# Performance work log

Measured on AMD Instinct MI355X. Metric: run time of the kernel, lower is better.

Reference implementation:

```python
import jax, jax.numpy as jnp
import numpy as np

FLOW_NUM = 2048
H = 64  # lstm_output_dim
NOISE_DIM = 3


def _w(key, shape, s=0.08):
    return (jax.random.normal(key, shape, dtype=jnp.float32) * s)


def setup_inputs() -> dict:
    key = jax.random.key(0)
    ks = jax.random.split(key, 20)
    d = {
        "noise": jax.random.normal(ks[0], (FLOW_NUM, NOISE_DIM), dtype=jnp.float32),
        "w_ih0": _w(ks[1], (4 * H, NOISE_DIM)),
        "w_hh0": _w(ks[2], (4 * H, H)),
        "b_ih0": _w(ks[3], (4 * H,)),
        "b_hh0": _w(ks[4], (4 * H,)),
        "w_ih1": _w(ks[5], (4 * H, H)),
        "w_hh1": _w(ks[6], (4 * H, H)),
        "b_ih1": _w(ks[7], (4 * H,)),
        "b_hh1": _w(ks[8], (4 * H,)),
        "w_ih2": _w(ks[9], (4 * H, H)),
        "w_hh2": _w(ks[10], (4 * H, H)),
        "b_ih2": _w(ks[11], (4 * H,)),
        "b_hh2": _w(ks[12], (4 * H,)),
        "fc1_w": _w(ks[13], (32, H)),
        "fc1_b": _w(ks[14], (32,)),
        "fc2_w": _w(ks[15], (16, 32)),
        "fc2_b": _w(ks[16], (16,)),
        "fc3_w": _w(ks[17], (3, 16)),
        "fc3_b": _w(ks[18], (3,)),
        "flow_length": 500,
    }
    return d


def _lstm_cell(x, h, c, w_ih, w_hh, b_ih, b_hh):
    # PyTorch gate order: input, forget, cell(g), output
    gates = x @ w_ih.T + h @ w_hh.T + (b_ih + b_hh)
    i, f, g, o = jnp.split(gates, 4, axis=-1)
    c_new = jax.nn.sigmoid(f) * c + jax.nn.sigmoid(i) * jnp.tanh(g)
    h_new = jax.nn.sigmoid(o) * jnp.tanh(c_new)
    return h_new, c_new


def reference(noise, w_ih0, w_hh0, b_ih0, b_hh0,
              w_ih1, w_hh1, b_ih1, b_hh1,
              w_ih2, w_hh2, b_ih2, b_hh2,
              fc1_w, fc1_b, fc2_w, fc2_b, fc3_w, fc3_b,
              flow_length):
    layers = [(w_ih0, w_hh0, b_ih0, b_hh0),
              (w_ih1, w_hh1, b_ih1, b_hh1),
              (w_ih2, w_hh2, b_ih2, b_hh2)]
    n = noise.shape[0]
    h0 = jnp.zeros((3, n, H), dtype=noise.dtype)
    c0 = jnp.zeros((3, n, H), dtype=noise.dtype)

    def step(carry, _):
        x, h, c = carry
        inp = x
        hs, cs = [], []
        for l, (wi, wh, bi, bh) in enumerate(layers):
            h_l, c_l = _lstm_cell(inp, h[l], c[l], wi, wh, bi, bh)
            hs.append(h_l)
            cs.append(c_l)
            inp = h_l
        # MLP head (Dropout is identity in eval mode); LeakyReLU slope 0.01
        y = jax.nn.leaky_relu(inp @ fc1_w.T + fc1_b)
        y = jax.nn.leaky_relu(y @ fc2_w.T + fc2_b)
        y = jax.nn.leaky_relu(y @ fc3_w.T + fc3_b)
        return (y, jnp.stack(hs), jnp.stack(cs)), y

    _, flow = jax.lax.scan(step, (noise, h0, c0), None, length=flow_length)
    # flow: [flow_length, flow_num, 3] -> [flow_num, flow_length, 3]
    return jnp.swapaxes(flow, 0, 1)
```

## Files before the change

### kernel.cpp

```cpp
#include <hip/hip_runtime.h>

#define NT 512

typedef _Float16 f16x8 __attribute__((ext_vector_type(8)));
typedef _Float16 f16x4 __attribute__((ext_vector_type(4)));
typedef float    f32x4 __attribute__((ext_vector_type(4)));

#define MFMA(a, b, c) __builtin_amdgcn_mfma_f32_16x16x32_f16((a), (b), (c), 0, 0, 0)

#if __has_builtin(__builtin_amdgcn_exp2f)
__device__ __forceinline__ float fexp(float x) { return __builtin_amdgcn_exp2f(x * 1.4426950408889634f); }
#else
__device__ __forceinline__ float fexp(float x) { return __expf(x); }
#endif
#if __has_builtin(__builtin_amdgcn_rcpf)
__device__ __forceinline__ float frcp(float x) { return __builtin_amdgcn_rcpf(x); }
#else
__device__ __forceinline__ float frcp(float x) { return 1.0f / x; }
#endif
__device__ __forceinline__ float sigm(float x)  { return frcp(1.0f + fexp(-x)); }
__device__ __forceinline__ float tanh_(float x) { return 1.0f - 2.0f * frcp(1.0f + fexp(2.0f * x)); }
__device__ __forceinline__ float lrelu(float x) { return x > 0.0f ? x : 0.01f * x; }

__device__ __forceinline__ f16x8 ld8(const float* p) {
    const float4* q = (const float4*)p;
    float4 a = q[0], b = q[1];
    f16x8 r = { (_Float16)a.x, (_Float16)a.y, (_Float16)a.z, (_Float16)a.w,
                (_Float16)b.x, (_Float16)b.y, (_Float16)b.z, (_Float16)b.w };
    return r;
}

__global__ __launch_bounds__(NT, 2)
void gen_kernel(
    const float* __restrict__ noise,
    const float* __restrict__ w_ih0, const float* __restrict__ w_hh0,
    const float* __restrict__ b_ih0, const float* __restrict__ b_hh0,
    const float* __restrict__ w_ih1, const float* __restrict__ w_hh1,
    const float* __restrict__ b_ih1, const float* __restrict__ b_hh1,
    const float* __restrict__ w_ih2, const float* __restrict__ w_hh2,
    const float* __restrict__ b_ih2, const float* __restrict__ b_hh2,
    const float* __restrict__ fc1_w, const float* __restrict__ fc1_b,
    const float* __restrict__ fc2_w, const float* __restrict__ fc2_b,
    const float* __restrict__ fc3_w, const float* __restrict__ fc3_b,
    const int*   __restrict__ flow_len_p,
    float* __restrict__ out)
{
    __shared__ _Float16 sh[3][2][16 * 64] __attribute__((aligned(16)));
    __shared__ _Float16 sx [16][40] __attribute__((aligned(16)));
    __shared__ _Float16 sy1[16][40] __attribute__((aligned(16)));
    __shared__ _Float16 sy2[16][40] __attribute__((aligned(16)));

    const int tid  = threadIdx.x;
    const int l    = tid & 63;
    const int w    = tid >> 6;
    const int ls   = l & 15;
    const int lj   = l >> 4;
    const int base = blockIdx.x * 8;
    const int T    = flow_len_p[0];

    const int gA  = ls & 3;
    const int rA0 = gA * 64 + 4 * (2 * w + 0) + (ls >> 2);
    const int rA1 = gA * 64 + 4 * (2 * w + 1) + (ls >> 2);

    f16x8 A1[2][4], A2[2][4], A0[2][3];
#pragma unroll
    for (int kc = 0; kc < 2; ++kc) {
        A1[0][kc]     = ld8(w_ih1 + rA0 * 64 + 32 * kc + 8 * lj);
        A1[1][kc]     = ld8(w_ih1 + rA1 * 64 + 32 * kc + 8 * lj);
        A1[0][2 + kc] = ld8(w_hh1 + rA0 * 64 + 32 * kc + 8 * lj);
        A1[1][2 + kc] = ld8(w_hh1 + rA1 * 64 + 32 * kc + 8 * lj);
        A2[0][kc]     = ld8(w_ih2 + rA0 * 64 + 32 * kc + 8 * lj);
        A2[1][kc]     = ld8(w_ih2 + rA1 * 64 + 32 * kc + 8 * lj);
        A2[0][2 + kc] = ld8(w_hh2 + rA0 * 64 + 32 * kc + 8 * lj);
        A2[1][2 + kc] = ld8(w_hh2 + rA1 * 64 + 32 * kc + 8 * lj);
        A0[0][kc]     = ld8(w_hh0 + rA0 * 64 + 32 * kc + 8 * lj);
        A0[1][kc]     = ld8(w_hh0 + rA1 * 64 + 32 * kc + 8 * lj);
    }
#pragma unroll
    for (int tt = 0; tt < 2; ++tt) {
        const int r = tt ? rA1 : rA0;
        f16x8 v;
#pragma unroll
        for (int i = 0; i < 8; ++i) {
            int kl = 8 * lj + i;
            float x = (kl < 3) ? w_ih0[r * 3 + kl]
                    : (kl == 3) ? (b_ih0[r] + b_hh0[r]) : 0.0f;
            v[i] = (_Float16)x;
        }
        A0[tt][2] = v;
    }
    f16x8 F1[2][2], F2, F3;
#pragma unroll
    for (int tt = 0; tt < 2; ++tt)
#pragma unroll
        for (int kc = 0; kc < 2; ++kc)
            F1[tt][kc] = ld8(fc1_w + (16 * tt + ls) * 64 + 32 * kc + 8 * lj);
    F2 = ld8(fc2_w + ls * 32 + 8 * lj);
    {
        f16x8 v;
#pragma unroll
        for (int i = 0; i < 8; ++i) {
            int k = 8 * lj + i;
            v[i] = (_Float16)((ls < 3 && k < 16) ? fc3_w[ls * 16 + k] : 0.0f);
        }
        F3 = v;
    }
    const int uc0 = 8 * w + lj, uc1 = 8 * w + 4 + lj;
    const int u_own = (ls < 8) ? uc0 : uc1;
    const int cs    = ls & 7;
    const int whaddr = cs * 64 + 8 * (((u_own >> 3) + cs) & 7) + (u_own & 7);
    float b1o[4], b2o[4];
#pragma unroll
    for (int g = 0; g < 4; ++g) {
        b1o[g] = b_ih1[g * 64 + u_own] + b_hh1[g * 64 + u_own];
        b2o[g] = b_ih2[g * 64 + u_own] + b_hh2[g * 64 + u_own];
    }
    float hb1a[4], hb1b[4], hb2[4];
#pragma unroll
    for (int r = 0; r < 4; ++r) {
        hb1a[r] = fc1_b[4 * lj + r];
        hb1b[r] = fc1_b[16 + 4 * lj + r];
        hb2[r]  = fc2_b[4 * lj + r];
    }
    float fb3[3] = { fc3_b[0], fc3_b[1], fc3_b[2] };

    for (int i = tid; i < 3 * 2 * 16 * 64; i += NT) ((_Float16*)sh)[i] = (_Float16)0.0f;
    for (int i = tid; i < 16 * 40; i += NT) {
        ((_Float16*)sx)[i]  = (_Float16)0.0f;
        ((_Float16*)sy1)[i] = (_Float16)0.0f;
        ((_Float16*)sy2)[i] = (_Float16)0.0f;
    }
    __syncthreads();
    if (tid < 16) sx[tid][3] = (_Float16)1.0f;
    if (tid < 24) {
        int s = tid / 3, d = tid % 3;
        sx[s][d] = (_Float16)noise[(base + s) * 3 + d];
    }

    float c0s = 0.0f, c1s = 0.0f, c2s = 0.0f;
    const float zb[4] = {0, 0, 0, 0};
    __syncthreads();

#define RD(L, p, kg) (*(const f16x8*)&sh[L][p][ls * 64 + 8 * (((kg) + ls) & 7)])

#define REPACK(cell, a0, a1)                                                   \
    float cell[4];                                                             \
    _Pragma("unroll")                                                          \
    for (int r = 0; r < 4; ++r) {                                              \
        float v_ = __shfl_xor(a1[r], 8);                                       \
        cell[r] = (ls < 8) ? a0[r] : v_;                                       \
    }

#define ACTC(cell, bo, cref, L, p) {                                           \
        float gi = cell[0] + bo[0], gf = cell[1] + bo[1];                      \
        float gg = cell[2] + bo[2], go = cell[3] + bo[3];                      \
        cref = sigm(gf) * cref + sigm(gi) * tanh_(gg);                         \
        sh[L][p][whaddr] = (_Float16)(sigm(go) * tanh_(cref)); }

    {
        f16x8 bx = *(const f16x8*)&sx[ls][8 * lj];
        f32x4 a0 = {0, 0, 0, 0}, a1 = {0, 0, 0, 0};
        a0 = MFMA(A0[0][2], bx, a0);
        a1 = MFMA(A0[1][2], bx, a1);
        REPACK(cell, a0, a1)
        ACTC(cell, zb, c0s, 0, 0)
    }
    __syncthreads();
    f16x8 ph1a = RD(1, 1, lj), ph1b = RD(1, 1, 4 + lj);

    for (int t = 0; t < T; ++t) {
        const int pc = t & 1, pp = pc ^ 1;
        f16x8 r0 = RD(0, pc, lj), r1 = RD(0, pc, 4 + lj);
        f16x8 nh2a = RD(2, pp, lj), nh2b = RD(2, pp, 4 + lj);
        {
            f32x4 a0 = {0, 0, 0, 0}, a1 = {0, 0, 0, 0};
            a0 = MFMA(A1[0][0], r0, a0);   a1 = MFMA(A1[1][0], r0, a1);
            a0 = MFMA(A1[0][1], r1, a0);   a1 = MFMA(A1[1][1], r1, a1);
            a0 = MFMA(A1[0][2], ph1a, a0); a1 = MFMA(A1[1][2], ph1a, a1);
            a0 = MFMA(A1[0][3], ph1b, a0); a1 = MFMA(A1[1][3], ph1b, a1);
            REPACK(cell, a0, a1)
            ACTC(cell, b1o, c1s, 1, pc)
        }
        __syncthreads();
        {
            f16x8 s0 = RD(1, pc, lj), s1 = RD(1, pc, 4 + lj);
            f32x4 a0 = {0, 0, 0, 0}, a1 = {0, 0, 0, 0};
            a0 = MFMA(A2[0][0], s0, a0);   a1 = MFMA(A2[1][0], s0, a1);
            a0 = MFMA(A2[0][1], s1, a0);   a1 = MFMA(A2[1][1], s1, a1);
            a0 = MFMA(A2[0][2], nh2a, a0); a1 = MFMA(A2[1][2], nh2a, a1);
            a0 = MFMA(A2[0][3], nh2b, a0); a1 = MFMA(A2[1][3], nh2b, a1);
            REPACK(cell, a0, a1)
            ACTC(cell, b2o, c2s, 2, pc)
        }
        __syncthreads();
        f32x4 h0a = {0, 0, 0, 0}, h0b = {0, 0, 0, 0};
        h0a = MFMA(A0[0][0], r0, h0a); h0b = MFMA(A0[1][0], r0, h0b);
        h0a = MFMA(A0[0][1], r1, h0a); h0b = MFMA(A0[1][1], r1, h0b);
        if (w == 0) {
            f16x8 bh0 = RD(2, pc, lj), bh1 = RD(2, pc, 4 + lj);
            f32x4 y1a = {0, 0, 0, 0}, y1b = {0, 0, 0, 0};
            y1a = MFMA(F1[0][0], bh0, y1a); y1b = MFMA(F1[1][0], bh0, y1b);
            y1a = MFMA(F1[0][1], bh1, y1a); y1b = MFMA(F1[1][1], bh1, y1b);
            f16x4 v;
#pragma unroll
            for (int r = 0; r < 4; ++r) v[r] = (_Float16)lrelu(y1a[r] + hb1a[r]);
            *(f16x4*)&sy1[ls][4 * lj] = v;
#pragma unroll
            for (int r = 0; r < 4; ++r) v[r] = (_Float16)lrelu(y1b[r] + hb1b[r]);
            *(f16x4*)&sy1[ls][16 + 4 * lj] = v;
            f16x8 by1 = *(const f16x8*)&sy1[ls][8 * lj];
            f32x4 y2 = {0, 0, 0, 0};
            y2 = MFMA(F2, by1, y2);
#pragma unroll
            for (int r = 0; r < 4; ++r) v[r] = (_Float16)lrelu(y2[r] + hb2[r]);
            *(f16x4*)&sy2[ls][4 * lj] = v;
            f16x8 by2 = *(const f16x8*)&sy2[ls][8 * lj];
            f32x4 y3 = {0, 0, 0, 0};
            y3 = MFMA(F3, by2, y3);
            if (lj == 0) {
                float o0 = lrelu(y3[0] + fb3[0]);
                float o1 = lrelu(y3[1] + fb3[1]);
                float o2 = lrelu(y3[2] + fb3[2]);
                sx[ls][0] = (_Float16)o0;
                sx[ls][1] = (_Float16)o1;
                sx[ls][2] = (_Float16)o2;
                if (ls < 8) {
                    float* op = out + ((size_t)(base + ls) * T + t) * 3;
                    op[0] = o0; op[1] = o1; op[2] = o2;
                }
            }
        }
        __syncthreads();
        {
            f16x8 bx = *(const f16x8*)&sx[ls][8 * lj];
            h0a = MFMA(A0[0][2], bx, h0a);
            h0b = MFMA(A0[1][2], bx, h0b);
            REPACK(cell, h0a, h0b)
            ACTC(cell, zb, c0s, 0, pp)
        }
        ph1a = RD(1, pc, lj); ph1b = RD(1, pc, 4 + lj);
        __syncthreads();
    }
}

extern "C" void kernel_launch(void* const* d_in, const int* in_sizes, int n_in,
                              void* d_out, int out_size, void* d_ws, size_t ws_size,
                              hipStream_t stream) {
    const float* noise = (const float*)d_in[0];
    const float* w_ih0 = (const float*)d_in[1];
    const float* w_hh0 = (const float*)d_in[2];
    const float* b_ih0 = (const float*)d_in[3];
    const float* b_hh0 = (const float*)d_in[4];
    const float* w_ih1 = (const float*)d_in[5];
    const float* w_hh1 = (const float*)d_in[6];
    const float* b_ih1 = (const float*)d_in[7];
    const float* b_hh1 = (const float*)d_in[8];
    const float* w_ih2 = (const float*)d_in[9];
    const float* w_hh2 = (const float*)d_in[10];
    const float* b_ih2 = (const float*)d_in[11];
    const float* b_hh2 = (const float*)d_in[12];
    const float* fc1w  = (const float*)d_in[13];
    const float* fc1b  = (const float*)d_in[14];
    const float* fc2w  = (const float*)d_in[15];
    const float* fc2b  = (const float*)d_in[16];
    const float* fc3w  = (const float*)d_in[17];
    const float* fc3b  = (const float*)d_in[18];
    const int*   flp   = (const int*)d_in[19];

    gen_kernel<<<dim3(256), dim3(NT), 0, stream>>>(
        noise, w_ih0, w_hh0, b_ih0, b_hh0,
        w_ih1, w_hh1, b_ih1, b_hh1,
        w_ih2, w_hh2, b_ih2, b_hh2,
        fc1w, fc1b, fc2w, fc2b, fc3w, fc3b,
        flp, (float*)d_out);
}
```

Measured before the change: 808.3 us.

## Replace MLP head LDS round-trips with cross-lane shuffles and unroll time loop by two

The MLP head on wave 0 used to write its fc1 and fc2 activations to shared memory and read them back as MFMA B-operands. That is now done with packed half shuffles inside the wave, so the sy1/sy2 buffers go away. The time loop is unrolled by two so the ping-pong buffer indices are constant, and the rotated LDS addresses are computed once before the loop. This removes LDS latency from the serial head path at the cost of shuffle instructions and larger code.

```diff
diff --git a/kernel.cpp b/kernel.cpp
--- a/kernel.cpp
+++ b/kernel.cpp
@@ -3,7 +3,6 @@
 #define NT 512
 
 typedef _Float16 f16x8 __attribute__((ext_vector_type(8)));
-typedef _Float16 f16x4 __attribute__((ext_vector_type(4)));
 typedef float    f32x4 __attribute__((ext_vector_type(4)));
 
 #define MFMA(a, b, c) __builtin_amdgcn_mfma_f32_16x16x32_f16((a), (b), (c), 0, 0, 0)
@@ -28,6 +27,13 @@
     f16x8 r = { (_Float16)a.x, (_Float16)a.y, (_Float16)a.z, (_Float16)a.w,
                 (_Float16)b.x, (_Float16)b.y, (_Float16)b.z, (_Float16)b.w };
     return r;
+}
+__device__ __forceinline__ unsigned pack2(float a, float b) {
+    union { _Float16 h[2]; unsigned u; } x;
+    x.h[0] = (_Float16)a; x.h[1] = (_Float16)b; return x.u;
+}
+__device__ __forceinline__ _Float16 half_of(unsigned v, int sel) {
+    union { unsigned u; _Float16 h[2]; } x; x.u = v; return x.h[sel];
 }
 
 __global__ __launch_bounds__(NT, 2)
@@ -46,9 +52,7 @@
     float* __restrict__ out)
 {
     __shared__ _Float16 sh[3][2][16 * 64] __attribute__((aligned(16)));
-    __shared__ _Float16 sx [16][40] __attribute__((aligned(16)));
-    __shared__ _Float16 sy1[16][40] __attribute__((aligned(16)));
-    __shared__ _Float16 sy2[16][40] __attribute__((aligned(16)));
+    __shared__ _Float16 sx[16][40] __attribute__((aligned(16)));
 
     const int tid  = threadIdx.x;
     const int l    = tid & 63;
@@ -124,12 +128,15 @@
     }
     float fb3[3] = { fc3_b[0], fc3_b[1], fc3_b[2] };
 
+    const int colb = ls * 64;
+    const int rot0 = colb + 8 * ((lj + ls) & 7);
+    const int rot1 = colb + 8 * ((4 + lj + ls) & 7);
+    const int sxoff = ls * 40 + 8 * lj;
+    const int laneA = ls + 32 * (lj & 1);
+    const int selH  = lj >> 1;
+
     for (int i = tid; i < 3 * 2 * 16 * 64; i += NT) ((_Float16*)sh)[i] = (_Float16)0.0f;
-    for (int i = tid; i < 16 * 40; i += NT) {
-        ((_Float16*)sx)[i]  = (_Float16)0.0f;
-        ((_Float16*)sy1)[i] = (_Float16)0.0f;
-        ((_Float16*)sy2)[i] = (_Float16)0.0f;
-    }
+    for (int i = tid; i < 16 * 40; i += NT) ((_Float16*)sx)[i] = (_Float16)0.0f;
     __syncthreads();
     if (tid < 16) sx[tid][3] = (_Float16)1.0f;
     if (tid < 24) {
@@ -141,7 +148,7 @@
     const float zb[4] = {0, 0, 0, 0};
     __syncthreads();
 
-#define RD(L, p, kg) (*(const f16x8*)&sh[L][p][ls * 64 + 8 * (((kg) + ls) & 7)])
+#define RDo(L, p, off) (*(const f16x8*)&sh[L][p][off])
 
 #define REPACK(cell, a0, a1)                                                   \
     float cell[4];                                                             \
@@ -158,7 +165,7 @@
         sh[L][p][whaddr] = (_Float16)(sigm(go) * tanh_(cref)); }
 
     {
-        f16x8 bx = *(const f16x8*)&sx[ls][8 * lj];
+        f16x8 bx = *(const f16x8*)((const _Float16*)sx + sxoff);
         f32x4 a0 = {0, 0, 0, 0}, a1 = {0, 0, 0, 0};
         a0 = MFMA(A0[0][2], bx, a0);
         a1 = MFMA(A0[1][2], bx, a1);
@@ -166,80 +173,105 @@
         ACTC(cell, zb, c0s, 0, 0)
     }
     __syncthreads();
-    f16x8 ph1a = RD(1, 1, lj), ph1b = RD(1, 1, 4 + lj);
-
-    for (int t = 0; t < T; ++t) {
-        const int pc = t & 1, pp = pc ^ 1;
-        f16x8 r0 = RD(0, pc, lj), r1 = RD(0, pc, 4 + lj);
-        f16x8 nh2a = RD(2, pp, lj), nh2b = RD(2, pp, 4 + lj);
-        {
-            f32x4 a0 = {0, 0, 0, 0}, a1 = {0, 0, 0, 0};
-            a0 = MFMA(A1[0][0], r0, a0);   a1 = MFMA(A1[1][0], r0, a1);
-            a0 = MFMA(A1[0][1], r1, a0);   a1 = MFMA(A1[1][1], r1, a1);
-            a0 = MFMA(A1[0][2], ph1a, a0); a1 = MFMA(A1[1][2], ph1a, a1);
-            a0 = MFMA(A1[0][3], ph1b, a0); a1 = MFMA(A1[1][3], ph1b, a1);
-            REPACK(cell, a0, a1)
-            ACTC(cell, b1o, c1s, 1, pc)
+    f16x8 ph1a = RDo(1, 1, rot0), ph1b = RDo(1, 1, rot1);
+
+#define STEPBODY(PC, PP, tt)                                                   \
+    {                                                                          \
+                                                                       \
+        f16x8 r0 = RDo(0, PC, rot0), r1 = RDo(0, PC, rot1);                    \
+        f16x8 nh2a = RDo(2, PP, rot0), nh2b = RDo(2, PP, rot1);                \
+        {                                                                      \
+            f32x4 a0 = {0, 0, 0, 0}, a1 = {0, 0, 0, 0};                        \
+            a0 = MFMA(A1[0][0], r0, a0);   a1 = MFMA(A1[1][0], r0, a1);        \
+            a0 = MFMA(A1[0][1], r1, a0);   a1 = MFMA(A1[1][1], r1, a1);        \
+            a0 = MFMA(A1[0][2], ph1a, a0); a1 = MFMA(A1[1][2], ph1a, a1);      \
+            a0 = MFMA(A1[0][3], ph1b, a0); a1 = MFMA(A1[1][3], ph1b, a1);      \
+            REPACK(cell, a0, a1)                                               \
+            ACTC(cell, b1o, c1s, 1, PC)                                        \
+        }                                                                      \
+        __syncthreads();                                                       \
+                                                                       \
+        {                                                                      \
+            f16x8 s0 = RDo(1, PC, rot0), s1 = RDo(1, PC, rot1);                \
+            f32x4 a0 = {0, 0, 0, 0}, a1 = {0, 0, 0, 0};                        \
+            a0 = MFMA(A2[0][0], s0, a0);   a1 = MFMA(A2[1][0], s0, a1);        \
+            a0 = MFMA(A2[0][1], s1, a0);   a1 = MFMA(A2[1][1], s1, a1);        \
+            a0 = MFMA(A2[0][2], nh2a, a0); a1 = MFMA(A2[1][2], nh2a, a1);      \
+            a0 = MFMA(A2[0][3], nh2b, a0); a1 = MFMA(A2[1][3], nh2b, a1);      \
+            REPACK(cell, a0, a1)                                               \
+            ACTC(cell, b2o, c2s, 2, PC)                                        \
+        }                                                                      \
+        __syncthreads();                                                       \
+              \
+        f32x4 h0a = {0, 0, 0, 0}, h0b = {0, 0, 0, 0};                          \
+        h0a = MFMA(A0[0][0], r0, h0a); h0b = MFMA(A0[1][0], r0, h0b);          \
+        h0a = MFMA(A0[0][1], r1, h0a); h0b = MFMA(A0[1][1], r1, h0b);          \
+        if (w == 0) {                                                          \
+            f16x8 bh0 = RDo(2, PC, rot0), bh1 = RDo(2, PC, rot1);              \
+            f32x4 y1a = {0, 0, 0, 0}, y1b = {0, 0, 0, 0};                      \
+            y1a = MFMA(F1[0][0], bh0, y1a); y1b = MFMA(F1[1][0], bh0, y1b);    \
+            y1a = MFMA(F1[0][1], bh1, y1a); y1b = MFMA(F1[1][1], bh1, y1b);    \
+            unsigned pk[4];                                                    \
+            _Pragma("unroll")                                                  \
+            for (int r = 0; r < 4; ++r)                                        \
+                pk[r] = pack2(lrelu(y1a[r] + hb1a[r]),                         \
+                              lrelu(y1b[r] + hb1b[r]));                        \
+            f16x8 by1;                                                         \
+            _Pragma("unroll")                                                  \
+            for (int i = 0; i < 4; ++i)                                        \
+                by1[i] = half_of((unsigned)__shfl((int)pk[i], laneA), selH);   \
+            _Pragma("unroll")                                                  \
+            for (int i = 0; i < 4; ++i)                                        \
+                by1[4 + i] = half_of((unsigned)__shfl((int)pk[i], laneA + 16), selH); \
+            f32x4 y2 = {0, 0, 0, 0};                                           \
+            y2 = MFMA(F2, by1, y2);                                            \
+            float y2r[4];                                                      \
+            _Pragma("unroll")                                                  \
+            for (int r = 0; r < 4; ++r) y2r[r] = lrelu(y2[r] + hb2[r]);        \
+            f16x8 by2;                                                         \
+            _Pragma("unroll")                                                  \
+            for (int i = 0; i < 4; ++i) {                                      \
+                float v_ = __shfl(y2r[i], laneA);                              \
+                by2[i] = (lj < 2) ? (_Float16)v_ : (_Float16)0.0f;             \
+            }                                                                  \
+            _Pragma("unroll")                                                  \
+            for (int i = 0; i < 4; ++i) {                                      \
+                float v_ = __shfl(y2r[i], laneA + 16);                         \
+                by2[4 + i] = (lj < 2) ? (_Float16)v_ : (_Float16)0.0f;         \
+            }                                                                  \
+            f32x4 y3 = {0, 0, 0, 0};                                           \
+            y3 = MFMA(F3, by2, y3);                                            \
+            if (lj == 0) {                                                     \
+                float o0 = lrelu(y3[0] + fb3[0]);                              \
+                float o1 = lrelu(y3[1] + fb3[1]);                              \
+                float o2 = lrelu(y3[2] + fb3[2]);                              \
+                sx[ls][0] = (_Float16)o0;                                      \
+                sx[ls][1] = (_Float16)o1;                                      \
+                sx[ls][2] = (_Float16)o2;                                      \
+                if (ls < 8) {                                                  \
+                    float* op = out + ((size_t)(base + ls) * T + (tt)) * 3;    \
+                    op[0] = o0; op[1] = o1; op[2] = o2;                        \
+                }                                                              \
+            }                                                                  \
+        }                                                                      \
+        __syncthreads();                                                       \
+                                                                       \
+        {                                                                      \
+            f16x8 bx = *(const f16x8*)((const _Float16*)sx + sxoff);           \
+            h0a = MFMA(A0[0][2], bx, h0a);                                     \
+            h0b = MFMA(A0[1][2], bx, h0b);                                     \
+            REPACK(cell, h0a, h0b)                                             \
+            ACTC(cell, zb, c0s, 0, PP)                                         \
+        }                                                                      \
+        ph1a = RDo(1, PC, rot0); ph1b = RDo(1, PC, rot1);                      \
+        __syncthreads();                                                       \
+    }
+
+    for (int t = 0; t < T; t += 2) {
+        STEPBODY(0, 1, t)
+        if (t + 1 < T) {
+            STEPBODY(1, 0, t + 1)
         }
-        __syncthreads();
-        {
-            f16x8 s0 = RD(1, pc, lj), s1 = RD(1, pc, 4 + lj);
-            f32x4 a0 = {0, 0, 0, 0}, a1 = {0, 0, 0, 0};
-            a0 = MFMA(A2[0][0], s0, a0);   a1 = MFMA(A2[1][0], s0, a1);
-            a0 = MFMA(A2[0][1], s1, a0);   a1 = MFMA(A2[1][1], s1, a1);
-            a0 = MFMA(A2[0][2], nh2a, a0); a1 = MFMA(A2[1][2], nh2a, a1);
-            a0 = MFMA(A2[0][3], nh2b, a0); a1 = MFMA(A2[1][3], nh2b, a1);
-            REPACK(cell, a0, a1)
-            ACTC(cell, b2o, c2s, 2, pc)
-        }
-        __syncthreads();
-        f32x4 h0a = {0, 0, 0, 0}, h0b = {0, 0, 0, 0};
-        h0a = MFMA(A0[0][0], r0, h0a); h0b = MFMA(A0[1][0], r0, h0b);
-        h0a = MFMA(A0[0][1], r1, h0a); h0b = MFMA(A0[1][1], r1, h0b);
-        if (w == 0) {
-            f16x8 bh0 = RD(2, pc, lj), bh1 = RD(2, pc, 4 + lj);
-            f32x4 y1a = {0, 0, 0, 0}, y1b = {0, 0, 0, 0};
-            y1a = MFMA(F1[0][0], bh0, y1a); y1b = MFMA(F1[1][0], bh0, y1b);
-            y1a = MFMA(F1[0][1], bh1, y1a); y1b = MFMA(F1[1][1], bh1, y1b);
-            f16x4 v;
-#pragma unroll
-            for (int r = 0; r < 4; ++r) v[r] = (_Float16)lrelu(y1a[r] + hb1a[r]);
-            *(f16x4*)&sy1[ls][4 * lj] = v;
-#pragma unroll
-            for (int r = 0; r < 4; ++r) v[r] = (_Float16)lrelu(y1b[r] + hb1b[r]);
-            *(f16x4*)&sy1[ls][16 + 4 * lj] = v;
-            f16x8 by1 = *(const f16x8*)&sy1[ls][8 * lj];
-            f32x4 y2 = {0, 0, 0, 0};
-            y2 = MFMA(F2, by1, y2);
-#pragma unroll
-            for (int r = 0; r < 4; ++r) v[r] = (_Float16)lrelu(y2[r] + hb2[r]);
-            *(f16x4*)&sy2[ls][4 * lj] = v;
-            f16x8 by2 = *(const f16x8*)&sy2[ls][8 * lj];
-            f32x4 y3 = {0, 0, 0, 0};
-            y3 = MFMA(F3, by2, y3);
-            if (lj == 0) {
-                float o0 = lrelu(y3[0] + fb3[0]);
-                float o1 = lrelu(y3[1] + fb3[1]);
-                float o2 = lrelu(y3[2] + fb3[2]);
-                sx[ls][0] = (_Float16)o0;
-                sx[ls][1] = (_Float16)o1;
-                sx[ls][2] = (_Float16)o2;
-                if (ls < 8) {
-                    float* op = out + ((size_t)(base + ls) * T + t) * 3;
-                    op[0] = o0; op[1] = o1; op[2] = o2;
-                }
-            }
-        }
-        __syncthreads();
-        {
-            f16x8 bx = *(const f16x8*)&sx[ls][8 * lj];
-            h0a = MFMA(A0[0][2], bx, h0a);
-            h0b = MFMA(A0[1][2], bx, h0b);
-            REPACK(cell, h0a, h0b)
-            ACTC(cell, zb, c0s, 0, pp)
-        }
-        ph1a = RD(1, pc, lj); ph1b = RD(1, pc, 4 + lj);
-        __syncthreads();
     }
 }
 
```

After: 865.4 us. 1.07x slower.

## Compute MLP head redundantly in every wave and drop a block barrier

Applied to the files above, without the earlier changes.

Each wave now computes the fc1/fc2/fc3 head itself, where before only wave 0 did it and passed results through shared memory. The layer outputs move between lanes with cross-lane shuffles instead of LDS staging. This removes one __syncthreads per timestep plus the sx/sy1/sy2 shared buffers, shortening the serial critical path of the recurrence. In exchange every wave repeats the head MFMAs and shuffles, which adds per-wave work.

```diff
diff --git a/kernel.cpp b/kernel.cpp
--- a/kernel.cpp
+++ b/kernel.cpp
@@ -3,7 +3,6 @@
 #define NT 512
 
 typedef _Float16 f16x8 __attribute__((ext_vector_type(8)));
-typedef _Float16 f16x4 __attribute__((ext_vector_type(4)));
 typedef float    f32x4 __attribute__((ext_vector_type(4)));
 
 #define MFMA(a, b, c) __builtin_amdgcn_mfma_f32_16x16x32_f16((a), (b), (c), 0, 0, 0)
@@ -28,6 +27,13 @@
     f16x8 r = { (_Float16)a.x, (_Float16)a.y, (_Float16)a.z, (_Float16)a.w,
                 (_Float16)b.x, (_Float16)b.y, (_Float16)b.z, (_Float16)b.w };
     return r;
+}
+__device__ __forceinline__ unsigned pack2(float a, float b) {
+    union { _Float16 h[2]; unsigned u; } x;
+    x.h[0] = (_Float16)a; x.h[1] = (_Float16)b; return x.u;
+}
+__device__ __forceinline__ _Float16 half_of(unsigned v, int sel) {
+    union { unsigned u; _Float16 h[2]; } x; x.u = v; return x.h[sel];
 }
 
 __global__ __launch_bounds__(NT, 2)
@@ -46,9 +52,6 @@
     float* __restrict__ out)
 {
     __shared__ _Float16 sh[3][2][16 * 64] __attribute__((aligned(16)));
-    __shared__ _Float16 sx [16][40] __attribute__((aligned(16)));
-    __shared__ _Float16 sy1[16][40] __attribute__((aligned(16)));
-    __shared__ _Float16 sy2[16][40] __attribute__((aligned(16)));
 
     const int tid  = threadIdx.x;
     const int l    = tid & 63;
@@ -123,19 +126,10 @@
         hb2[r]  = fc2_b[4 * lj + r];
     }
     float fb3[3] = { fc3_b[0], fc3_b[1], fc3_b[2] };
+    const int laneA = ls + 32 * (lj & 1);
+    const int selH  = lj >> 1;
 
     for (int i = tid; i < 3 * 2 * 16 * 64; i += NT) ((_Float16*)sh)[i] = (_Float16)0.0f;
-    for (int i = tid; i < 16 * 40; i += NT) {
-        ((_Float16*)sx)[i]  = (_Float16)0.0f;
-        ((_Float16*)sy1)[i] = (_Float16)0.0f;
-        ((_Float16*)sy2)[i] = (_Float16)0.0f;
-    }
-    __syncthreads();
-    if (tid < 16) sx[tid][3] = (_Float16)1.0f;
-    if (tid < 24) {
-        int s = tid / 3, d = tid % 3;
-        sx[s][d] = (_Float16)noise[(base + s) * 3 + d];
-    }
 
     float c0s = 0.0f, c1s = 0.0f, c2s = 0.0f;
     const float zb[4] = {0, 0, 0, 0};
@@ -158,7 +152,17 @@
         sh[L][p][whaddr] = (_Float16)(sigm(go) * tanh_(cref)); }
 
     {
-        f16x8 bx = *(const f16x8*)&sx[ls][8 * lj];
+        f16x8 bx;
+#pragma unroll
+        for (int i = 0; i < 8; ++i) bx[i] = (_Float16)0.0f;
+        if (lj == 0) {
+            if (ls < 8) {
+                bx[0] = (_Float16)noise[(base + ls) * 3 + 0];
+                bx[1] = (_Float16)noise[(base + ls) * 3 + 1];
+                bx[2] = (_Float16)noise[(base + ls) * 3 + 2];
+            }
+            bx[3] = (_Float16)1.0f;
+        }
         f32x4 a0 = {0, 0, 0, 0}, a1 = {0, 0, 0, 0};
         a0 = MFMA(A0[0][2], bx, a0);
         a1 = MFMA(A0[1][2], bx, a1);
@@ -193,46 +197,59 @@
             ACTC(cell, b2o, c2s, 2, pc)
         }
         __syncthreads();
-        f32x4 h0a = {0, 0, 0, 0}, h0b = {0, 0, 0, 0};
-        h0a = MFMA(A0[0][0], r0, h0a); h0b = MFMA(A0[1][0], r0, h0b);
-        h0a = MFMA(A0[0][1], r1, h0a); h0b = MFMA(A0[1][1], r1, h0b);
-        if (w == 0) {
+        {
+            f32x4 h0a = {0, 0, 0, 0}, h0b = {0, 0, 0, 0};
+            h0a = MFMA(A0[0][0], r0, h0a); h0b = MFMA(A0[1][0], r0, h0b);
+            h0a = MFMA(A0[0][1], r1, h0a); h0b = MFMA(A0[1][1], r1, h0b);
+
             f16x8 bh0 = RD(2, pc, lj), bh1 = RD(2, pc, 4 + lj);
             f32x4 y1a = {0, 0, 0, 0}, y1b = {0, 0, 0, 0};
-            y1a = MFMA(F1[0][0], bh0, y1a); y1b = MFMA(F1[1][0], bh0, y1b);
-            y1a = MFMA(F1[0][1], bh1, y1a); y1b = MFMA(F1[1][1], bh1, y1b);
-            f16x4 v;
-#pragma unroll
-            for (int r = 0; r < 4; ++r) v[r] = (_Float16)lrelu(y1a[r] + hb1a[r]);
-            *(f16x4*)&sy1[ls][4 * lj] = v;
-#pragma unroll
-            for (int r = 0; r < 4; ++r) v[r] = (_Float16)lrelu(y1b[r] + hb1b[r]);
-            *(f16x4*)&sy1[ls][16 + 4 * lj] = v;
-            f16x8 by1 = *(const f16x8*)&sy1[ls][8 * lj];
+            y1a = MFMA(F1[0][0], bh0, y1a); y1a = MFMA(F1[0][1], bh1, y1a);
+            y1b = MFMA(F1[1][0], bh0, y1b); y1b = MFMA(F1[1][1], bh1, y1b);
+            unsigned pk[4];
+#pragma unroll
+            for (int r = 0; r < 4; ++r)
+                pk[r] = pack2(lrelu(y1a[r] + hb1a[r]), lrelu(y1b[r] + hb1b[r]));
+            f16x8 by1;
+#pragma unroll
+            for (int i = 0; i < 4; ++i)
+                by1[i] = half_of((unsigned)__shfl((int)pk[i], laneA), selH);
+#pragma unroll
+            for (int i = 0; i < 4; ++i)
+                by1[4 + i] = half_of((unsigned)__shfl((int)pk[i], laneA + 16), selH);
             f32x4 y2 = {0, 0, 0, 0};
             y2 = MFMA(F2, by1, y2);
-#pragma unroll
-            for (int r = 0; r < 4; ++r) v[r] = (_Float16)lrelu(y2[r] + hb2[r]);
-            *(f16x4*)&sy2[ls][4 * lj] = v;
-            f16x8 by2 = *(const f16x8*)&sy2[ls][8 * lj];
+            float y2r[4];
+#pragma unroll
+            for (int r = 0; r < 4; ++r) y2r[r] = lrelu(y2[r] + hb2[r]);
+            f16x8 by2;
+#pragma unroll
+            for (int i = 0; i < 4; ++i) {
+                float v_ = __shfl(y2r[i], laneA);
+                by2[i] = (lj < 2) ? (_Float16)v_ : (_Float16)0.0f;
+            }
+#pragma unroll
+            for (int i = 0; i < 4; ++i) {
+                float v_ = __shfl(y2r[i], laneA + 16);
+                by2[4 + i] = (lj < 2) ? (_Float16)v_ : (_Float16)0.0f;
+            }
             f32x4 y3 = {0, 0, 0, 0};
             y3 = MFMA(F3, by2, y3);
+
+            f16x8 bx;
+#pragma unroll
+            for (int i = 0; i < 8; ++i) bx[i] = (_Float16)0.0f;
             if (lj == 0) {
                 float o0 = lrelu(y3[0] + fb3[0]);
                 float o1 = lrelu(y3[1] + fb3[1]);
                 float o2 = lrelu(y3[2] + fb3[2]);
-                sx[ls][0] = (_Float16)o0;
-                sx[ls][1] = (_Float16)o1;
-                sx[ls][2] = (_Float16)o2;
-                if (ls < 8) {
+                bx[0] = (_Float16)o0; bx[1] = (_Float16)o1;
+                bx[2] = (_Float16)o2; bx[3] = (_Float16)1.0f;
+                if (w == 0 && ls < 8) {
                     float* op = out + ((size_t)(base + ls) * T + t) * 3;
                     op[0] = o0; op[1] = o1; op[2] = o2;
                 }
             }
-        }
-        __syncthreads();
-        {
-            f16x8 bx = *(const f16x8*)&sx[ls][8 * lj];
             h0a = MFMA(A0[0][2], bx, h0a);
             h0b = MFMA(A0[1][2], bx, h0b);
             REPACK(cell, h0a, h0b)
```

Result: slower. 1.030 ms (+27.5%).
